# Optimization experiments

Measured on AMD Instinct MI355X. Metric: run time of the kernel, lower is better.

Reference implementation:

```python
import jax, jax.numpy as jnp
import numpy as np

N_EMBED = 2048
N_HEAD = 16
HEAD_SIZE = N_EMBED // N_HEAD  # 128


def rotate_half(x):
    x1, x2 = jnp.split(x, 2, axis=-1)
    return jnp.concatenate((-x2, x1), axis=-1)


def setup_inputs() -> dict:
    key = jax.random.key(0)
    k_x, k_qkv, k_proj, k_b = jax.random.split(key, 4)
    B, T = 4, 2048
    x = jax.random.normal(k_x, (B, T, N_EMBED), dtype=jnp.float32)
    # weights stored as [in, out] so y = x @ W (equivalent param'n of nn.Linear)
    w_qkv = jax.random.normal(k_qkv, (N_EMBED, 3 * N_EMBED), dtype=jnp.float32) * (N_EMBED ** -0.5)
    w_proj = jax.random.normal(k_proj, (N_EMBED, N_EMBED), dtype=jnp.float32) * (N_EMBED ** -0.5)
    b_proj = jax.random.normal(k_b, (N_EMBED,), dtype=jnp.float32) * 0.02
    return {"x": x, "w_qkv": w_qkv, "w_proj": w_proj, "b_proj": b_proj}


def reference(x, w_qkv, w_proj, b_proj):
    B, T, C = x.shape
    H, D = N_HEAD, HEAD_SIZE
    qkv = x @ w_qkv                                   # [B,T,3C]
    q, k, v = jnp.split(qkv, 3, axis=2)
    q = q.reshape(B, T, H, D).transpose(0, 2, 1, 3)   # [B,H,T,D]
    k = k.reshape(B, T, H, D).transpose(0, 2, 1, 3)
    v = v.reshape(B, T, H, D).transpose(0, 2, 1, 3)
    # RoPE in fp32
    inv_freq = 1.0 / (10000.0 ** (jnp.arange(0, D, 2, dtype=jnp.float32) / D))
    t = jnp.arange(T, dtype=jnp.float32)
    freqs = jnp.einsum('i,j->ij', t, inv_freq)        # [T,D/2]
    emb = jnp.concatenate((freqs, freqs), axis=-1)    # [T,D]
    cos = jnp.cos(emb)[None, None, :, :]
    sin = jnp.sin(emb)[None, None, :, :]
    qf = q.astype(jnp.float32)
    kf = k.astype(jnp.float32)
    q = (qf * cos + rotate_half(qf) * sin).astype(v.dtype)
    k = (kf * cos + rotate_half(kf) * sin).astype(v.dtype)
    # causal SDPA
    scale = 1.0 / jnp.sqrt(jnp.asarray(D, dtype=q.dtype))
    scores = jnp.einsum('bhqd,bhkd->bhqk', q, k) * scale
    causal = jnp.tril(jnp.ones((T, T), dtype=bool))
    scores = jnp.where(causal[None, None, :, :], scores, jnp.finfo(scores.dtype).min)
    attn = jax.nn.softmax(scores, axis=-1)
    out = jnp.einsum('bhqk,bhkd->bhqd', attn, v)      # [B,H,T,D]
    out = out.transpose(0, 2, 1, 3).reshape(B, T, C)
    return out @ w_proj + b_proj
```

## Files before the change

kernel.cpp:

```cpp
#include <hip/hip_runtime.h>
#include <hip/hip_bf16.h>
#include <cstdint>
#include <cstddef>

typedef __bf16 bf16x8 __attribute__((ext_vector_type(8)));
typedef __bf16 bf16x4 __attribute__((ext_vector_type(4)));
typedef float  f32x4  __attribute__((ext_vector_type(4)));

__device__ __forceinline__ void lds_load16(const void* gsrc, void* ldst) {
    __builtin_amdgcn_global_load_lds(
        (const __attribute__((address_space(1))) unsigned int*)gsrc,
        (__attribute__((address_space(3))) unsigned int*)ldst,
        16, 0, 0);
}

__global__ __launch_bounds__(256) void cvt_k(const float* __restrict__ in,
                                             __bf16* __restrict__ out, int n8) {
    int i = blockIdx.x * 256 + threadIdx.x;
    if (i >= n8) return;
    const float4* p4 = (const float4*)in + (size_t)i * 2;
    float4 a = p4[0], b = p4[1];
    bf16x8 o;
    o[0] = (__bf16)a.x; o[1] = (__bf16)a.y; o[2] = (__bf16)a.z; o[3] = (__bf16)a.w;
    o[4] = (__bf16)b.x; o[5] = (__bf16)b.y; o[6] = (__bf16)b.z; o[7] = (__bf16)b.w;
    *((bf16x8*)out + i) = o;
}

__global__ __launch_bounds__(256) void transp_k(const float* __restrict__ W,
                                                __bf16* __restrict__ WT, int R, int C) {
    __shared__ float tile[32][33];
    int tx = threadIdx.x & 31, ty = threadIdx.x >> 5;
    int c0 = blockIdx.x * 32, r0 = blockIdx.y * 32;
#pragma unroll
    for (int k = 0; k < 4; ++k)
        tile[ty + 8 * k][tx] = W[(size_t)(r0 + ty + 8 * k) * C + c0 + tx];
    __syncthreads();
#pragma unroll
    for (int k = 0; k < 4; ++k)
        WT[(size_t)(c0 + ty + 8 * k) * R + r0 + tx] = (__bf16)tile[tx][ty + 8 * k];
}

__global__ __launch_bounds__(256) void sincos_k(float2* __restrict__ sc) {
    int idx = blockIdx.x * 256 + threadIdx.x;
    int t = idx >> 6, j = idx & 63;
    float inv = powf(10000.f, -(float)j / 64.f);
    float f = (float)t * inv;
    float s, c;
    sincosf(f, &s, &c);
    sc[idx] = make_float2(c, s);
}

__global__ __launch_bounds__(256) void rope_k(__bf16* __restrict__ qb, __bf16* __restrict__ kb,
                                              const float2* __restrict__ sc) {
    unsigned idx = blockIdx.x * 256 + threadIdx.x;
    int tensor = idx >> 20;
    unsigned i = idx & 0xFFFFFu;
    int jb = (i & 7) * 8;
    int t = (i >> 3) & 2047;
    int bh = i >> 14;
    __bf16* p = tensor ? kb : qb;
    size_t base = ((size_t)bh * 2048 + t) * 128;
    bf16x8 lo = *(bf16x8*)(p + base + jb);
    bf16x8 hi = *(bf16x8*)(p + base + 64 + jb);
    const float2* s2 = sc + t * 64 + jb;
    float scale = tensor ? 1.f : 0.08838834764831845f;
    bf16x8 olo, ohi;
#pragma unroll
    for (int e = 0; e < 8; ++e) {
        float c = s2[e].x, s = s2[e].y;
        float x1 = (float)lo[e], x2 = (float)hi[e];
        olo[e] = (__bf16)((x1 * c - x2 * s) * scale);
        ohi[e] = (__bf16)((x2 * c + x1 * s) * scale);
    }
    *(bf16x8*)(p + base + jb) = olo;
    *(bf16x8*)(p + base + 64 + jb) = ohi;
}

__global__ __launch_bounds__(512, 2) void gemm8_k(const __bf16* __restrict__ A,
                                                  const __bf16* __restrict__ Bt,
                                                  int nbn, int mode,
                                                  __bf16* __restrict__ qb, __bf16* __restrict__ kb,
                                                  __bf16* __restrict__ vt,
                                                  float* __restrict__ outp,
                                                  const float* __restrict__ bias) {
    __shared__ __bf16 lds[2][2][2][128 * 64];
    const int K = 2048, NT = K / 64;
    int nwg = gridDim.x;
    int per = nwg >> 3;
    int bid = blockIdx.x;
    int wg = (bid & 7) * per + (bid >> 3);
    int bm = wg / nbn, bn = wg % nbn;
    int m0 = bm * 256, n0 = bn * 256;
    int tid = threadIdx.x;
    int lane = tid & 63, wave = tid >> 6;
    int wm = wave >> 2, wn = wave & 3;
    int lr = lane & 15, lg = lane >> 4;

    f32x4 acc[8][4] = {};

    auto stageA = [&](int db, int sub, int kt) {
#pragma unroll
        for (int l = 0; l < 2; ++l) {
            int chunk = l * 512 + tid;
            int r = chunk >> 3, c16 = chunk & 7;
            int rg = m0 + ((r >> 6) << 7) + (sub << 6) + (r & 63);
            lds_load16(A + (size_t)rg * K + (kt << 6) + ((c16 ^ (r & 7)) << 3),
                       &lds[db][0][sub][chunk * 8]);
        }
    };
    auto stageB = [&](int db, int sub, int kt) {
#pragma unroll
        for (int l = 0; l < 2; ++l) {
            int chunk = l * 512 + tid;
            int r = chunk >> 3, c16 = chunk & 7;
            int rg = n0 + ((r >> 5) << 6) + (sub << 5) + (r & 31);
            lds_load16(Bt + (size_t)rg * K + (kt << 6) + ((c16 ^ (r & 7)) << 3),
                       &lds[db][1][sub][chunk * 8]);
        }
    };
    auto rdA = [&](int db, int sub, int q, int kk) -> bf16x8 {
        int r = (wm << 6) + (q << 4) + lr;
        int cb = ((kk << 6) + (lg << 4)) ^ ((r & 7) << 4);
        return *(const bf16x8*)((const char*)&lds[db][0][sub][0] + r * 128 + cb);
    };
    auto rdB = [&](int db, int j, int kk) -> bf16x8 {
        int sub = j >> 1;
        int r = (wn << 5) + ((j & 1) << 4) + lr;
        int cb = ((kk << 6) + (lg << 4)) ^ ((r & 7) << 4);
        return *(const bf16x8*)((const char*)&lds[db][1][sub][0] + r * 128 + cb);
    };

    stageA(0, 0, 0); stageB(0, 0, 0); stageB(0, 1, 0); stageA(0, 1, 0);
    asm volatile("s_waitcnt vmcnt(0)" ::: "memory");
    __builtin_amdgcn_s_barrier();

    bf16x8 a[4][2], b0[2][2], b1[2][2];
    for (int t = 0; t < NT; ++t) {
        int db = t & 1, dn = db ^ 1;
        bool pf = (t + 1 < NT);
#pragma unroll
        for (int q = 0; q < 4; ++q) { a[q][0] = rdA(db, 0, q, 0); a[q][1] = rdA(db, 0, q, 1); }
#pragma unroll
        for (int j = 0; j < 2; ++j) { b0[j][0] = rdB(db, j, 0); b0[j][1] = rdB(db, j, 1); }
        if (pf) stageA(dn, 0, t + 1);
        asm volatile("s_waitcnt vmcnt(4)" ::: "memory");
        __builtin_amdgcn_s_barrier();
        asm volatile("s_waitcnt lgkmcnt(0)" ::: "memory");
        __builtin_amdgcn_sched_barrier(0);
        __builtin_amdgcn_s_setprio(1);
#pragma unroll
        for (int q = 0; q < 4; ++q)
#pragma unroll
            for (int j = 0; j < 2; ++j)
#pragma unroll
                for (int kk = 0; kk < 2; ++kk)
                    acc[q][j] = __builtin_amdgcn_mfma_f32_16x16x32_bf16(a[q][kk], b0[j][kk], acc[q][j], 0, 0, 0);
        __builtin_amdgcn_s_setprio(0);
        __builtin_amdgcn_s_barrier();
#pragma unroll
        for (int j = 0; j < 2; ++j) { b1[j][0] = rdB(db, j + 2, 0); b1[j][1] = rdB(db, j + 2, 1); }
        if (pf) stageB(dn, 0, t + 1);
        asm volatile("s_waitcnt vmcnt(4)" ::: "memory");
        __builtin_amdgcn_s_barrier();
        asm volatile("s_waitcnt lgkmcnt(0)" ::: "memory");
        __builtin_amdgcn_sched_barrier(0);
        __builtin_amdgcn_s_setprio(1);
#pragma unroll
        for (int q = 0; q < 4; ++q)
#pragma unroll
            for (int j = 0; j < 2; ++j)
#pragma unroll
                for (int kk = 0; kk < 2; ++kk)
                    acc[q][j + 2] = __builtin_amdgcn_mfma_f32_16x16x32_bf16(a[q][kk], b1[j][kk], acc[q][j + 2], 0, 0, 0);
        __builtin_amdgcn_s_setprio(0);
        __builtin_amdgcn_s_barrier();
#pragma unroll
        for (int q = 0; q < 4; ++q) { a[q][0] = rdA(db, 1, q, 0); a[q][1] = rdA(db, 1, q, 1); }
        if (pf) stageB(dn, 1, t + 1);
        asm volatile("s_waitcnt vmcnt(4)" ::: "memory");
        __builtin_amdgcn_s_barrier();
        asm volatile("s_waitcnt lgkmcnt(0)" ::: "memory");
        __builtin_amdgcn_sched_barrier(0);
        __builtin_amdgcn_s_setprio(1);
#pragma unroll
        for (int q = 0; q < 4; ++q)
#pragma unroll
            for (int j = 0; j < 2; ++j)
#pragma unroll
                for (int kk = 0; kk < 2; ++kk)
                    acc[q + 4][j + 2] = __builtin_amdgcn_mfma_f32_16x16x32_bf16(a[q][kk], b1[j][kk], acc[q + 4][j + 2], 0, 0, 0);
        __builtin_amdgcn_s_setprio(0);
        __builtin_amdgcn_s_barrier();
        if (pf) stageA(dn, 1, t + 1);
        asm volatile("s_waitcnt vmcnt(4)" ::: "memory");
        __builtin_amdgcn_s_barrier();
        __builtin_amdgcn_sched_barrier(0);
        __builtin_amdgcn_s_setprio(1);
#pragma unroll
        for (int q = 0; q < 4; ++q)
#pragma unroll
            for (int j = 0; j < 2; ++j)
#pragma unroll
                for (int kk = 0; kk < 2; ++kk)
                    acc[q + 4][j] = __builtin_amdgcn_mfma_f32_16x16x32_bf16(a[q][kk], b0[j][kk], acc[q + 4][j], 0, 0, 0);
        __builtin_amdgcn_s_setprio(0);
        __builtin_amdgcn_s_barrier();
    }

    if (mode == 0) {
#pragma unroll
        for (int q = 0; q < 8; ++q) {
            int row_t = (wm << 7) + ((q >> 2) << 6) + ((q & 3) << 4) + (lg << 2);
#pragma unroll
            for (int j = 0; j < 4; ++j) {
                int c = n0 + (wn << 6) + (j << 4) + lr;
                int which = c >> 11;
                int h = (c & 2047) >> 7;
                int d = c & 127;
#pragma unroll
                for (int r = 0; r < 4; ++r) {
                    int row = m0 + row_t + r;
                    int b_ = row >> 11, tt = row & 2047;
                    __bf16 val = (__bf16)acc[q][j][r];
                    size_t bh = (size_t)(b_ * 16 + h);
                    if (which == 0)      qb[(bh * 2048 + tt) * 128 + d] = val;
                    else if (which == 1) kb[(bh * 2048 + tt) * 128 + d] = val;
                    else                 vt[(bh * 128 + d) * 2048 + tt] = val;
                }
            }
        }
    } else {
#pragma unroll
        for (int q = 0; q < 8; ++q) {
            int row_t = (wm << 7) + ((q >> 2) << 6) + ((q & 3) << 4) + (lg << 2);
#pragma unroll
            for (int j = 0; j < 4; ++j) {
                int col = n0 + (wn << 6) + (j << 4) + lr;
                float bv = bias[col];
#pragma unroll
                for (int r = 0; r < 4; ++r) {
                    int row = m0 + row_t + r;
                    outp[(size_t)row * 2048 + col] = acc[q][j][r] + bv;
                }
            }
        }
    }
}

__global__ __launch_bounds__(256, 2) void attn_k(const __bf16* __restrict__ qb,
                                                 const __bf16* __restrict__ kb,
                                                 const __bf16* __restrict__ vt,
                                                 __bf16* __restrict__ ao) {
    __shared__ __bf16 Ks[64 * 128];
    __shared__ __bf16 Vs[128 * 64];
    __shared__ __bf16 Ps[4][16 * 64];

    int bid = blockIdx.x;
    int qt = 31 - (bid >> 6);
    int bh = bid & 63;
    int qs = qt * 64;
    int tid = threadIdx.x, wave = tid >> 6, lane = tid & 63;
    int lr = lane & 15, lg = lane >> 4;

    bf16x8 qf[4];
    const __bf16* Qrow = qb + ((size_t)bh * 2048 + qs + wave * 16 + lr) * 128;
#pragma unroll
    for (int kk = 0; kk < 4; ++kk) qf[kk] = *(const bf16x8*)(Qrow + kk * 32 + lg * 8);

    f32x4 ot[8] = {};
    float m_run = -1e30f, l_run = 0.f;

    for (int ks = 0; ks <= qs; ks += 64) {
#pragma unroll
        for (int i = 0; i < 4; ++i) {
            int c = tid + i * 256;
            {
                int row = c >> 4;
                int cc = c ^ (row & 7);
                int dd = (cc & 15) * 8;
                lds_load16(kb + ((size_t)bh * 2048 + ks + row) * 128 + dd, Ks + c * 8);
            }
            {
                int row = c >> 3;
                int cc = c ^ (row & 7);
                int tt = (cc & 7) * 8;
                lds_load16(vt + ((size_t)bh * 128 + row) * 2048 + ks + tt, Vs + c * 8);
            }
        }
        __syncthreads();

        f32x4 st[4];
#pragma unroll
        for (int mt = 0; mt < 4; ++mt) {
            f32x4 s = {};
#pragma unroll
            for (int kk = 0; kk < 4; ++kk) {
                int row = mt * 16 + lr;
                const __bf16* kp = Ks + row * 128 + ((((kk * 64 + lg * 16)) ^ ((row & 7) << 4)) >> 1);
                bf16x8 afr = *(const bf16x8*)kp;
                s = __builtin_amdgcn_mfma_f32_16x16x32_bf16(afr, qf[kk], s, 0, 0, 0);
            }
            st[mt] = s;
        }

        if (ks == qs) {
            int q = qs + wave * 16 + lr;
#pragma unroll
            for (int mt = 0; mt < 4; ++mt)
#pragma unroll
                for (int r = 0; r < 4; ++r) {
                    int kv = ks + mt * 16 + lg * 4 + r;
                    if (kv > q) st[mt][r] = -1e30f;
                }
        }

        float pm = -1e30f;
#pragma unroll
        for (int mt = 0; mt < 4; ++mt)
#pragma unroll
            for (int r = 0; r < 4; ++r) pm = fmaxf(pm, st[mt][r]);
        pm = fmaxf(pm, __shfl_xor(pm, 16));
        pm = fmaxf(pm, __shfl_xor(pm, 32));
        float nm = fmaxf(m_run, pm);
        float alpha = __expf(m_run - nm);
        float psum = 0.f;
#pragma unroll
        for (int mt = 0; mt < 4; ++mt)
#pragma unroll
            for (int r = 0; r < 4; ++r) {
                float p = __expf(st[mt][r] - nm);
                psum += p;
                st[mt][r] = p;
            }
        psum += __shfl_xor(psum, 16);
        psum += __shfl_xor(psum, 32);
        l_run = l_run * alpha + psum;
        m_run = nm;
#pragma unroll
        for (int t8 = 0; t8 < 8; ++t8) ot[t8] *= alpha;

#pragma unroll
        for (int mt = 0; mt < 4; ++mt) {
            bf16x4 pk;
#pragma unroll
            for (int r = 0; r < 4; ++r) pk[r] = (__bf16)st[mt][r];
            int byteoff = lr * 128 + (((mt * 32 + lg * 8)) ^ ((lr & 7) << 4));
            *(bf16x4*)((char*)&Ps[wave][0] + byteoff) = pk;
        }

        bf16x8 pfr[2];
#pragma unroll
        for (int kk = 0; kk < 2; ++kk) {
            const char* pp = (const char*)&Ps[wave][0] + lr * 128 + (((kk * 64 + lg * 16)) ^ ((lr & 7) << 4));
            pfr[kk] = *(const bf16x8*)pp;
        }
#pragma unroll
        for (int dt = 0; dt < 8; ++dt) {
#pragma unroll
            for (int kk = 0; kk < 2; ++kk) {
                int row = dt * 16 + lr;
                const __bf16* vp = Vs + row * 64 + ((((kk * 64 + lg * 16)) ^ ((row & 7) << 4)) >> 1);
                bf16x8 afr = *(const bf16x8*)vp;
                ot[dt] = __builtin_amdgcn_mfma_f32_16x16x32_bf16(afr, pfr[kk], ot[dt], 0, 0, 0);
            }
        }
        __syncthreads();
    }

    float inv = 1.f / l_run;
    int b_ = bh >> 4, h = bh & 15;
    size_t rowbase = ((size_t)b_ * 2048 + qs + wave * 16 + lr) * 2048 + h * 128;
#pragma unroll
    for (int dt = 0; dt < 8; ++dt) {
        bf16x4 o;
#pragma unroll
        for (int r = 0; r < 4; ++r) o[r] = (__bf16)(ot[dt][r] * inv);
        *(bf16x4*)(ao + rowbase + dt * 16 + lg * 4) = o;
    }
}

extern "C" void kernel_launch(void* const* d_in, const int* in_sizes, int n_in,
                              void* d_out, int out_size, void* d_ws, size_t ws_size,
                              hipStream_t stream) {
    const float* x      = (const float*)d_in[0];
    const float* w_qkv  = (const float*)d_in[1];
    const float* w_proj = (const float*)d_in[2];
    const float* b_proj = (const float*)d_in[3];
    float* out = (float*)d_out;
    char* ws = (char*)d_ws;

    __bf16* xb  = (__bf16*)(ws);
    __bf16* wqt = (__bf16*)(ws + 33554432);
    __bf16* wpt = (__bf16*)(ws + 58720256);
    __bf16* qb  = (__bf16*)(ws + 67108864);
    __bf16* kb  = (__bf16*)(ws + 100663296);
    __bf16* vt  = (__bf16*)(ws + 134217728);
    __bf16* ao  = (__bf16*)(ws + 167772160);
    float2* sc  = (float2*)(ws + 201326592);

    hipLaunchKernelGGL(cvt_k, dim3(8192), dim3(256), 0, stream, x, xb, 2097152);
    hipLaunchKernelGGL(transp_k, dim3(192, 64), dim3(256), 0, stream, w_qkv, wqt, 2048, 6144);
    hipLaunchKernelGGL(transp_k, dim3(64, 64), dim3(256), 0, stream, w_proj, wpt, 2048, 2048);
    hipLaunchKernelGGL(sincos_k, dim3(512), dim3(256), 0, stream, sc);
    hipLaunchKernelGGL(gemm8_k, dim3(768), dim3(512), 0, stream,
                       xb, wqt, 24, 0, qb, kb, vt, (float*)nullptr, (const float*)nullptr);
    hipLaunchKernelGGL(rope_k, dim3(8192), dim3(256), 0, stream, qb, kb, sc);
    hipLaunchKernelGGL(attn_k, dim3(2048), dim3(256), 0, stream, qb, kb, vt, ao);
    hipLaunchKernelGGL(gemm8_k, dim3(256), dim3(512), 0, stream,
                       ao, wpt, 8, 1, (__bf16*)nullptr, (__bf16*)nullptr, (__bf16*)nullptr,
                       out, b_proj);
}
```

Before: 453.2 us.

## Fuse RoPE into QKV GEMM epilogue, retime GEMM waits, raise MFMA priority

Drops the separate rope_k kernel. The QKV GEMM epilogue now applies rotary embedding and the Q scale by exchanging half-head columns through LDS scratch before the bf16 store, which removes a full read-modify-write pass over Q and K. The GEMM main loop also moves its vmcnt waits to after the MFMA blocks, cutting one barrier per sub-step so global loads overlap more with compute. The attention kernel additionally raises wave priority around its MFMA loops. In exchange the epilogue gains LDS round-trips and syncthreads, and the loosened wait counts risk races.

```diff
diff --git a/kernel.cpp b/kernel.cpp
--- a/kernel.cpp
+++ b/kernel.cpp
@@ -50,39 +50,14 @@
     sc[idx] = make_float2(c, s);
 }
 
-__global__ __launch_bounds__(256) void rope_k(__bf16* __restrict__ qb, __bf16* __restrict__ kb,
-                                              const float2* __restrict__ sc) {
-    unsigned idx = blockIdx.x * 256 + threadIdx.x;
-    int tensor = idx >> 20;
-    unsigned i = idx & 0xFFFFFu;
-    int jb = (i & 7) * 8;
-    int t = (i >> 3) & 2047;
-    int bh = i >> 14;
-    __bf16* p = tensor ? kb : qb;
-    size_t base = ((size_t)bh * 2048 + t) * 128;
-    bf16x8 lo = *(bf16x8*)(p + base + jb);
-    bf16x8 hi = *(bf16x8*)(p + base + 64 + jb);
-    const float2* s2 = sc + t * 64 + jb;
-    float scale = tensor ? 1.f : 0.08838834764831845f;
-    bf16x8 olo, ohi;
-#pragma unroll
-    for (int e = 0; e < 8; ++e) {
-        float c = s2[e].x, s = s2[e].y;
-        float x1 = (float)lo[e], x2 = (float)hi[e];
-        olo[e] = (__bf16)((x1 * c - x2 * s) * scale);
-        ohi[e] = (__bf16)((x2 * c + x1 * s) * scale);
-    }
-    *(bf16x8*)(p + base + jb) = olo;
-    *(bf16x8*)(p + base + 64 + jb) = ohi;
-}
-
 __global__ __launch_bounds__(512, 2) void gemm8_k(const __bf16* __restrict__ A,
                                                   const __bf16* __restrict__ Bt,
                                                   int nbn, int mode,
                                                   __bf16* __restrict__ qb, __bf16* __restrict__ kb,
                                                   __bf16* __restrict__ vt,
                                                   float* __restrict__ outp,
-                                                  const float* __restrict__ bias) {
+                                                  const float* __restrict__ bias,
+                                                  const float2* __restrict__ sc) {
     __shared__ __bf16 lds[2][2][2][128 * 64];
     const int K = 2048, NT = K / 64;
     int nwg = gridDim.x;
@@ -131,19 +106,18 @@
     };
 
     stageA(0, 0, 0); stageB(0, 0, 0); stageB(0, 1, 0); stageA(0, 1, 0);
-    asm volatile("s_waitcnt vmcnt(0)" ::: "memory");
+    asm volatile("s_waitcnt vmcnt(4)" ::: "memory");
     __builtin_amdgcn_s_barrier();
 
-    bf16x8 a[4][2], b0[2][2], b1[2][2];
+    bf16x8 a[4][2], bA[2][2], bB[2][2];
     for (int t = 0; t < NT; ++t) {
         int db = t & 1, dn = db ^ 1;
         bool pf = (t + 1 < NT);
 #pragma unroll
         for (int q = 0; q < 4; ++q) { a[q][0] = rdA(db, 0, q, 0); a[q][1] = rdA(db, 0, q, 1); }
 #pragma unroll
-        for (int j = 0; j < 2; ++j) { b0[j][0] = rdB(db, j, 0); b0[j][1] = rdB(db, j, 1); }
+        for (int j = 0; j < 2; ++j) { bA[j][0] = rdB(db, j, 0); bA[j][1] = rdB(db, j, 1); }
         if (pf) stageA(dn, 0, t + 1);
-        asm volatile("s_waitcnt vmcnt(4)" ::: "memory");
         __builtin_amdgcn_s_barrier();
         asm volatile("s_waitcnt lgkmcnt(0)" ::: "memory");
         __builtin_amdgcn_sched_barrier(0);
@@ -154,13 +128,14 @@
             for (int j = 0; j < 2; ++j)
 #pragma unroll
                 for (int kk = 0; kk < 2; ++kk)
-                    acc[q][j] = __builtin_amdgcn_mfma_f32_16x16x32_bf16(a[q][kk], b0[j][kk], acc[q][j], 0, 0, 0);
-        __builtin_amdgcn_s_setprio(0);
-        __builtin_amdgcn_s_barrier();
-#pragma unroll
-        for (int j = 0; j < 2; ++j) { b1[j][0] = rdB(db, j + 2, 0); b1[j][1] = rdB(db, j + 2, 1); }
+                    acc[q][j] = __builtin_amdgcn_mfma_f32_16x16x32_bf16(a[q][kk], bA[j][kk], acc[q][j], 0, 0, 0);
+        __builtin_amdgcn_s_setprio(0);
+        if (pf) asm volatile("s_waitcnt vmcnt(4)" ::: "memory");
+        else    asm volatile("s_waitcnt vmcnt(2)" ::: "memory");
+        __builtin_amdgcn_s_barrier();
+#pragma unroll
+        for (int j = 0; j < 2; ++j) { bB[j][0] = rdB(db, j + 2, 0); bB[j][1] = rdB(db, j + 2, 1); }
         if (pf) stageB(dn, 0, t + 1);
-        asm volatile("s_waitcnt vmcnt(4)" ::: "memory");
         __builtin_amdgcn_s_barrier();
         asm volatile("s_waitcnt lgkmcnt(0)" ::: "memory");
         __builtin_amdgcn_sched_barrier(0);
@@ -171,13 +146,14 @@
             for (int j = 0; j < 2; ++j)
 #pragma unroll
                 for (int kk = 0; kk < 2; ++kk)
-                    acc[q][j + 2] = __builtin_amdgcn_mfma_f32_16x16x32_bf16(a[q][kk], b1[j][kk], acc[q][j + 2], 0, 0, 0);
-        __builtin_amdgcn_s_setprio(0);
+                    acc[q][j + 2] = __builtin_amdgcn_mfma_f32_16x16x32_bf16(a[q][kk], bB[j][kk], acc[q][j + 2], 0, 0, 0);
+        __builtin_amdgcn_s_setprio(0);
+        if (pf) asm volatile("s_waitcnt vmcnt(4)" ::: "memory");
+        else    asm volatile("s_waitcnt vmcnt(0)" ::: "memory");
         __builtin_amdgcn_s_barrier();
 #pragma unroll
         for (int q = 0; q < 4; ++q) { a[q][0] = rdA(db, 1, q, 0); a[q][1] = rdA(db, 1, q, 1); }
         if (pf) stageB(dn, 1, t + 1);
-        asm volatile("s_waitcnt vmcnt(4)" ::: "memory");
         __builtin_amdgcn_s_barrier();
         asm volatile("s_waitcnt lgkmcnt(0)" ::: "memory");
         __builtin_amdgcn_sched_barrier(0);
@@ -188,13 +164,10 @@
             for (int j = 0; j < 2; ++j)
 #pragma unroll
                 for (int kk = 0; kk < 2; ++kk)
-                    acc[q + 4][j + 2] = __builtin_amdgcn_mfma_f32_16x16x32_bf16(a[q][kk], b1[j][kk], acc[q + 4][j + 2], 0, 0, 0);
+                    acc[q + 4][j + 2] = __builtin_amdgcn_mfma_f32_16x16x32_bf16(a[q][kk], bB[j][kk], acc[q + 4][j + 2], 0, 0, 0);
         __builtin_amdgcn_s_setprio(0);
         __builtin_amdgcn_s_barrier();
         if (pf) stageA(dn, 1, t + 1);
-        asm volatile("s_waitcnt vmcnt(4)" ::: "memory");
-        __builtin_amdgcn_s_barrier();
-        __builtin_amdgcn_sched_barrier(0);
         __builtin_amdgcn_s_setprio(1);
 #pragma unroll
         for (int q = 0; q < 4; ++q)
@@ -202,31 +175,63 @@
             for (int j = 0; j < 2; ++j)
 #pragma unroll
                 for (int kk = 0; kk < 2; ++kk)
-                    acc[q + 4][j] = __builtin_amdgcn_mfma_f32_16x16x32_bf16(a[q][kk], b0[j][kk], acc[q + 4][j], 0, 0, 0);
-        __builtin_amdgcn_s_setprio(0);
+                    acc[q + 4][j] = __builtin_amdgcn_mfma_f32_16x16x32_bf16(a[q][kk], bA[j][kk], acc[q + 4][j], 0, 0, 0);
+        __builtin_amdgcn_s_setprio(0);
+        if (pf) asm volatile("s_waitcnt vmcnt(4)" ::: "memory");
         __builtin_amdgcn_s_barrier();
     }
 
     if (mode == 0) {
-#pragma unroll
-        for (int q = 0; q < 8; ++q) {
-            int row_t = (wm << 7) + ((q >> 2) << 6) + ((q & 3) << 4) + (lg << 2);
-#pragma unroll
-            for (int j = 0; j < 4; ++j) {
-                int c = n0 + (wn << 6) + (j << 4) + lr;
-                int which = c >> 11;
-                int h = (c & 2047) >> 7;
-                int d = c & 127;
-#pragma unroll
-                for (int r = 0; r < 4; ++r) {
-                    int row = m0 + row_t + r;
-                    int b_ = row >> 11, tt = row & 2047;
-                    __bf16 val = (__bf16)acc[q][j][r];
-                    size_t bh = (size_t)(b_ * 16 + h);
-                    if (which == 0)      qb[(bh * 2048 + tt) * 128 + d] = val;
-                    else if (which == 1) kb[(bh * 2048 + tt) * 128 + d] = val;
-                    else                 vt[(bh * 128 + d) * 2048 + tt] = val;
+        int which = n0 >> 11;
+        if (which == 2) {
+#pragma unroll
+            for (int q = 0; q < 8; ++q) {
+                int row_t = (wm << 7) + ((q >> 2) << 6) + ((q & 3) << 4) + (lg << 2);
+#pragma unroll
+                for (int j = 0; j < 4; ++j) {
+                    int c = n0 + (wn << 6) + (j << 4) + lr;
+                    int h = (c & 2047) >> 7, d = c & 127;
+#pragma unroll
+                    for (int r = 0; r < 4; ++r) {
+                        int row = m0 + row_t + r;
+                        int b_ = row >> 11, tt = row & 2047;
+                        vt[((size_t)(b_ * 16 + h) * 128 + d) * 2048 + tt] = (__bf16)acc[q][j][r];
+                    }
                 }
+            }
+        } else {
+            __bf16* dst = (which == 0) ? qb : kb;
+            float scale = (which == 0) ? 0.08838834764831845f : 1.f;
+            float* scr = (float*)&lds[0][0][0][0];
+            int rl = (wm << 4) + (lg << 2);
+            int colw = (wn << 6);
+#pragma unroll
+            for (int q = 0; q < 8; ++q) {
+                int row_t = (wm << 7) + ((q >> 2) << 6) + ((q & 3) << 4) + (lg << 2);
+#pragma unroll
+                for (int j = 0; j < 4; ++j)
+#pragma unroll
+                    for (int r = 0; r < 4; ++r)
+                        scr[(rl + r) * 260 + colw + (j << 4) + lr] = acc[q][j][r];
+                __syncthreads();
+#pragma unroll
+                for (int j = 0; j < 4; ++j) {
+                    int c = n0 + colw + (j << 4) + lr;
+                    int h = (c & 2047) >> 7, d = c & 127;
+                    int jj = (j << 4) + lr;
+#pragma unroll
+                    for (int r = 0; r < 4; ++r) {
+                        int row = m0 + row_t + r;
+                        int b_ = row >> 11, tt = row & 2047;
+                        float2 cs = sc[tt * 64 + jj];
+                        float v0 = acc[q][j][r];
+                        float v1 = scr[(rl + r) * 260 + (colw ^ 64) + (j << 4) + lr];
+                        float o = ((wn & 1) == 0) ? (v0 * cs.x - v1 * cs.y)
+                                                  : (v0 * cs.x + v1 * cs.y);
+                        dst[((size_t)(b_ * 16 + h) * 2048 + tt) * 128 + d] = (__bf16)(o * scale);
+                    }
+                }
+                __syncthreads();
             }
         }
     } else {
@@ -290,6 +295,7 @@
         __syncthreads();
 
         f32x4 st[4];
+        __builtin_amdgcn_s_setprio(1);
 #pragma unroll
         for (int mt = 0; mt < 4; ++mt) {
             f32x4 s = {};
@@ -302,6 +308,7 @@
             }
             st[mt] = s;
         }
+        __builtin_amdgcn_s_setprio(0);
 
         if (ks == qs) {
             int q = qs + wave * 16 + lr;
@@ -354,6 +361,7 @@
             const char* pp = (const char*)&Ps[wave][0] + lr * 128 + (((kk * 64 + lg * 16)) ^ ((lr & 7) << 4));
             pfr[kk] = *(const bf16x8*)pp;
         }
+        __builtin_amdgcn_s_setprio(1);
 #pragma unroll
         for (int dt = 0; dt < 8; ++dt) {
 #pragma unroll
@@ -364,6 +372,7 @@
                 ot[dt] = __builtin_amdgcn_mfma_f32_16x16x32_bf16(afr, pfr[kk], ot[dt], 0, 0, 0);
             }
         }
+        __builtin_amdgcn_s_setprio(0);
         __syncthreads();
     }
 
@@ -403,10 +412,9 @@
     hipLaunchKernelGGL(transp_k, dim3(64, 64), dim3(256), 0, stream, w_proj, wpt, 2048, 2048);
     hipLaunchKernelGGL(sincos_k, dim3(512), dim3(256), 0, stream, sc);
     hipLaunchKernelGGL(gemm8_k, dim3(768), dim3(512), 0, stream,
-                       xb, wqt, 24, 0, qb, kb, vt, (float*)nullptr, (const float*)nullptr);
-    hipLaunchKernelGGL(rope_k, dim3(8192), dim3(256), 0, stream, qb, kb, sc);
+                       xb, wqt, 24, 0, qb, kb, vt, (float*)nullptr, (const float*)nullptr, sc);
     hipLaunchKernelGGL(attn_k, dim3(2048), dim3(256), 0, stream, qb, kb, vt, ao);
     hipLaunchKernelGGL(gemm8_k, dim3(256), dim3(512), 0, stream,
                        ao, wpt, 8, 1, (__bf16*)nullptr, (__bf16*)nullptr, (__bf16*)nullptr,
-                       out, b_proj);
-}
+                       out, b_proj, (const float2*)nullptr);
+}
```

Result: faster. 407.7 us (-10.0%).
